# Performance work log

Hardware: AMD Instinct MI355X
Metric: run time of the kernel (lower is better)

## Reference

```python
import jax, jax.numpy as jnp
import numpy as np

B, S, D, K, N = 4, 4096, 768, 24, 8192

def setup_inputs() -> dict:
    key = jax.random.key(0)
    k1, k2, k3, k4 = jax.random.split(key, 4)
    x = jax.random.normal(k1, (B, S, D), dtype=jnp.float32)
    phi = jax.random.normal(k2, (S, K), dtype=jnp.float32)
    M_inputs = jax.random.normal(k3, (D, D), dtype=jnp.float32) / np.sqrt(D)
    M_filters = jax.random.normal(k4, (K, D), dtype=jnp.float32) / np.sqrt(K)
    return {"x": x, "phi": phi, "M_inputs": M_inputs, "M_filters": M_filters, "n": N}


def reference(x, phi, M_inputs, M_filters, n):
    # STU.forward with use_approx=True, use_flash_fft=False
    bsz, sl, d = x.shape
    x_proj = x @ M_inputs               # [B, S, D]
    phi_proj = phi @ M_filters          # [S, D]
    # alternating sign sequence for the 'minus' spectral branch
    sgn = jnp.ones((1, sl, 1), dtype=x.dtype).at[:, 1::2].set(-1.0)
    # filters: [1, S, D, 1] broadcast over the plus/minus stack
    v = phi_proj[None, :, :, None]
    V = jnp.fft.rfft(v, n=n, axis=1)    # [1, n//2+1, D, 1] complex
    U = jnp.stack([x_proj, x_proj * sgn], axis=-1)  # [B, S, D, 2]
    Uf = jnp.fft.rfft(U, n=n, axis=1)   # [B, n//2+1, D, 2]
    U_conv = jnp.fft.irfft(V * Uf, n=n, axis=1)[:, :sl]  # [B, S, D, 2]
    spectral_plus = U_conv[..., 0]
    spectral_minus = U_conv[..., 1] * sgn
    return spectral_plus + spectral_minus
```

## Files before the change

### kernel.cpp

```cpp
#include <hip/hip_runtime.h>
#include <hip/hip_bf16.h>


#define NB 4
#define NS 4096
#define ND 768
#define NK 24

typedef __attribute__((ext_vector_type(8))) short short8;
typedef __attribute__((ext_vector_type(4))) float f32x4;
typedef __attribute__((ext_vector_type(4))) unsigned short u16x4;

static __device__ __forceinline__ float bf2f(unsigned short u) {
  union { unsigned int i; float f; } v; v.i = ((unsigned int)u) << 16; return v.f;
}
static __device__ __forceinline__ unsigned short f2bf(float f) {
  union { float f; unsigned int i; } v; v.f = f;
  return (unsigned short)((v.i + 0x7fffu + ((v.i >> 16) & 1u)) >> 16);
}

__device__ __forceinline__ float2 cadd(float2 a, float2 b){ return make_float2(a.x+b.x, a.y+b.y); }
__device__ __forceinline__ float2 csub(float2 a, float2 b){ return make_float2(a.x-b.x, a.y-b.y); }
__device__ __forceinline__ float2 cmul(float2 a, float2 b){ return make_float2(a.x*b.x-a.y*b.y, a.x*b.y+a.y*b.x); }
__device__ __forceinline__ float2 cmulc(float2 a, float2 b){ return make_float2(a.x*b.x+a.y*b.y, a.y*b.x-a.x*b.y); }

#define C4 0.70710678118654752f
#define C8 0.92387953251128674f
#define S8 0.38268343236508977f
#define TWO_PI 6.28318530717958648f

__device__ __forceinline__ void fft16_dif(float2 v[16]) {
  const float twr[8] = {1.f, C8, C4, S8, 0.f, -S8, -C4, -C8};
  const float twi[8] = {0.f, -S8, -C4, -C8, -1.f, -C8, -C4, -S8};
#pragma unroll
  for (int i = 0; i < 8; ++i) {
    float2 a = v[i], b = v[i+8];
    v[i] = cadd(a, b);
    float2 d = csub(a, b);
    v[i+8] = make_float2(d.x*twr[i]-d.y*twi[i], d.x*twi[i]+d.y*twr[i]);
  }
#pragma unroll
  for (int blk = 0; blk < 16; blk += 8)
#pragma unroll
    for (int i = 0; i < 4; ++i) {
      float2 a = v[blk+i], b = v[blk+i+4];
      v[blk+i] = cadd(a, b);
      float2 d = csub(a, b);
      v[blk+i+4] = make_float2(d.x*twr[2*i]-d.y*twi[2*i], d.x*twi[2*i]+d.y*twr[2*i]);
    }
#pragma unroll
  for (int blk = 0; blk < 16; blk += 4) {
    { float2 a = v[blk],   b = v[blk+2]; v[blk] = cadd(a,b);   v[blk+2] = csub(a,b); }
    { float2 a = v[blk+1], b = v[blk+3]; float2 d = csub(a,b);
      v[blk+1] = cadd(a,b); v[blk+3] = make_float2(d.y, -d.x); }
  }
#pragma unroll
  for (int blk = 0; blk < 16; blk += 2) {
    float2 a = v[blk], b = v[blk+1];
    v[blk] = cadd(a, b); v[blk+1] = csub(a, b);
  }
}

__device__ __forceinline__ void fft16_dif_zero8(float2 v[16]) {
  const float twr[8] = {1.f, C8, C4, S8, 0.f, -S8, -C4, -C8};
  const float twi[8] = {0.f, -S8, -C4, -C8, -1.f, -C8, -C4, -S8};
#pragma unroll
  for (int i = 1; i < 8; ++i) {
    float2 a = v[i];
    v[i+8] = make_float2(a.x*twr[i]-a.y*twi[i], a.x*twi[i]+a.y*twr[i]);
  }
  v[8] = v[0];
#pragma unroll
  for (int blk = 0; blk < 16; blk += 8)
#pragma unroll
    for (int i = 0; i < 4; ++i) {
      float2 a = v[blk+i], b = v[blk+i+4];
      v[blk+i] = cadd(a, b);
      float2 d = csub(a, b);
      v[blk+i+4] = make_float2(d.x*twr[2*i]-d.y*twi[2*i], d.x*twi[2*i]+d.y*twr[2*i]);
    }
#pragma unroll
  for (int blk = 0; blk < 16; blk += 4) {
    { float2 a = v[blk],   b = v[blk+2]; v[blk] = cadd(a,b);   v[blk+2] = csub(a,b); }
    { float2 a = v[blk+1], b = v[blk+3]; float2 d = csub(a,b);
      v[blk+1] = cadd(a,b); v[blk+3] = make_float2(d.y, -d.x); }
  }
#pragma unroll
  for (int blk = 0; blk < 16; blk += 2) {
    float2 a = v[blk], b = v[blk+1];
    v[blk] = cadd(a, b); v[blk+1] = csub(a, b);
  }
}

__device__ __forceinline__ void idft16(float2 v[16]) {
  const float twr[8] = {1.f, C8, C4, S8, 0.f, -S8, -C4, -C8};
  const float twi[8] = {0.f, S8, C4, C8, 1.f, C8, C4, S8};
#pragma unroll
  for (int blk = 0; blk < 16; blk += 2) {
    float2 a = v[blk], b = v[blk+1];
    v[blk] = cadd(a, b); v[blk+1] = csub(a, b);
  }
#pragma unroll
  for (int blk = 0; blk < 16; blk += 4) {
    { float2 a = v[blk],   b = v[blk+2]; v[blk] = cadd(a,b);   v[blk+2] = csub(a,b); }
    { float2 a = v[blk+1], b = v[blk+3]; float2 t = make_float2(-b.y, b.x);
      v[blk+1] = cadd(a,t); v[blk+3] = csub(a,t); }
  }
#pragma unroll
  for (int blk = 0; blk < 16; blk += 8)
#pragma unroll
    for (int i = 0; i < 4; ++i) {
      float2 b = v[blk+i+4];
      float2 t = make_float2(b.x*twr[2*i]-b.y*twi[2*i], b.x*twi[2*i]+b.y*twr[2*i]);
      float2 a = v[blk+i];
      v[blk+i] = cadd(a, t); v[blk+i+4] = csub(a, t);
    }
#pragma unroll
  for (int i = 0; i < 8; ++i) {
    float2 b = v[i+8];
    float2 t = make_float2(b.x*twr[i]-b.y*twi[i], b.x*twi[i]+b.y*twr[i]);
    float2 a = v[i];
    v[i] = cadd(a, t); v[i+8] = csub(a, t);
  }
}

__device__ __forceinline__ void idft16_low8(float2 v[16]) {
  const float twr[8] = {1.f, C8, C4, S8, 0.f, -S8, -C4, -C8};
  const float twi[8] = {0.f, S8, C4, C8, 1.f, C8, C4, S8};
#pragma unroll
  for (int blk = 0; blk < 16; blk += 2) {
    float2 a = v[blk], b = v[blk+1];
    v[blk] = cadd(a, b); v[blk+1] = csub(a, b);
  }
#pragma unroll
  for (int blk = 0; blk < 16; blk += 4) {
    { float2 a = v[blk],   b = v[blk+2]; v[blk] = cadd(a,b);   v[blk+2] = csub(a,b); }
    { float2 a = v[blk+1], b = v[blk+3]; float2 t = make_float2(-b.y, b.x);
      v[blk+1] = cadd(a,t); v[blk+3] = csub(a,t); }
  }
#pragma unroll
  for (int blk = 0; blk < 16; blk += 8)
#pragma unroll
    for (int i = 0; i < 4; ++i) {
      float2 b = v[blk+i+4];
      float2 t = make_float2(b.x*twr[2*i]-b.y*twi[2*i], b.x*twi[2*i]+b.y*twr[2*i]);
      float2 a = v[blk+i];
      v[blk+i] = cadd(a, t); v[blk+i+4] = csub(a, t);
    }
#pragma unroll
  for (int i = 0; i < 8; ++i) {
    float2 b = v[i+8];
    float2 t = make_float2(b.x*twr[i]-b.y*twi[i], b.x*twi[i]+b.y*twr[i]);
    v[i] = cadd(v[i], t);
  }
}

#define BR_TABLE {0,8,4,12,2,10,6,14,1,9,5,13,3,11,7,15}
#define PAD(i) ((i) + ((i) >> 4))

__global__ __launch_bounds__(256) void cast_x_bf16(const float* __restrict__ in,
                                                   unsigned short* __restrict__ out) {
  int i = (blockIdx.x * 256 + threadIdx.x) * 4;
  float4 v = *(const float4*)(in + i);
  u16x4 o = { f2bf(v.x), f2bf(v.y), f2bf(v.z), f2bf(v.w) };
  *(u16x4*)(out + i) = o;
}

__global__ __launch_bounds__(256) void transpose_cast_Mi(const float* __restrict__ Mi,
                                                         unsigned short* __restrict__ MiT) {
  __shared__ float tile[64][65];
  const int d0 = blockIdx.x * 64;
  const int e0 = blockIdx.y * 64;
  const int tid = threadIdx.x;
#pragma unroll
  for (int i = 0; i < 16; ++i) {
    int ee = (tid >> 6) + i * 4;
    int dd = tid & 63;
    tile[ee][dd] = Mi[(e0 + ee) * ND + d0 + dd];
  }
  __syncthreads();
#pragma unroll
  for (int i = 0; i < 8; ++i) {
    int dd = (tid >> 5) + i * 8;
    int ee2 = (tid & 31) * 2;
    unsigned int w = (unsigned int)f2bf(tile[ee2][dd]) |
                     ((unsigned int)f2bf(tile[ee2 + 1][dd]) << 16);
    *(unsigned int*)(MiT + (size_t)(d0 + dd) * ND + e0 + ee2) = w;
  }
}

__global__ __launch_bounds__(256) void gemm_xprojT(const unsigned short* __restrict__ Xb,
                                                   const unsigned short* __restrict__ MiT,
                                                   unsigned short* __restrict__ XPT) {
  __shared__ __align__(16) unsigned char smem[33792];
  unsigned short* As = (unsigned short*)smem;
  unsigned short* Bs = As + 128 * 32;
  const int tid = threadIdx.x;
  const int lane = tid & 63;
  const int wave = tid >> 6;
  const int c0 = blockIdx.x * 128;
  const int r0 = blockIdx.y * 128;
  const int wr = (wave >> 1) * 64;
  const int wc = (wave & 1) * 64;

  f32x4 acc[4][4];
#pragma unroll
  for (int m = 0; m < 4; ++m)
#pragma unroll
    for (int n = 0; n < 4; ++n) acc[m][n] = (f32x4){0.f, 0.f, 0.f, 0.f};

  const int ldRow = (lane >> 2);
  const int ldK = (lane & 3) * 8;

  for (int k0 = 0; k0 < ND; k0 += 32) {
    if (k0) __syncthreads();
#pragma unroll
    for (int h = 0; h < 2; ++h) {
      int c = wave * 2 + h;
      int row = c * 16 + ldRow;
      const unsigned short* ga = Xb + (size_t)(r0 + row) * ND + k0 + ldK;
      const unsigned short* gb = MiT + (size_t)(c0 + row) * ND + k0 + ldK;
      __builtin_amdgcn_global_load_lds(
          (const __attribute__((address_space(1))) void*)ga,
          (__attribute__((address_space(3))) void*)(As + c * 512), 16, 0, 0);
      __builtin_amdgcn_global_load_lds(
          (const __attribute__((address_space(1))) void*)gb,
          (__attribute__((address_space(3))) void*)(Bs + c * 512), 16, 0, 0);
    }
    __syncthreads();

    short8 a[4], b[4];
#pragma unroll
    for (int m = 0; m < 4; ++m)
      a[m] = *(const short8*)(As + (wr + m * 16 + (lane & 15)) * 32 + (lane >> 4) * 8);
#pragma unroll
    for (int n = 0; n < 4; ++n)
      b[n] = *(const short8*)(Bs + (wc + n * 16 + (lane & 15)) * 32 + (lane >> 4) * 8);
#pragma unroll
    for (int m = 0; m < 4; ++m)
#pragma unroll
      for (int n = 0; n < 4; ++n)
        acc[m][n] = __builtin_amdgcn_mfma_f32_16x16x32_bf16(a[m], b[n], acc[m][n], 0, 0, 0);
  }

  __syncthreads();
  unsigned int* Cb = (unsigned int*)smem;
#pragma unroll
  for (int m = 0; m < 4; ++m)
#pragma unroll
    for (int n = 0; n < 4; ++n) {
      int col = wc + n * 16 + (lane & 15);
      int sp = (wr + m * 16 + (lane >> 4) * 4) >> 1;
      f32x4 a4 = acc[m][n];
      unsigned int w0 = (unsigned int)f2bf(a4[0]) | ((unsigned int)f2bf(a4[1]) << 16);
      unsigned int w1 = (unsigned int)f2bf(a4[2]) | ((unsigned int)f2bf(a4[3]) << 16);
      *(uint2*)(Cb + col * 66 + sp) = make_uint2(w0, w1);
    }
  __syncthreads();
  const int bI = r0 >> 12;
  const int sBase = r0 & (NS - 1);
  {
    int col = tid >> 1, half = tid & 1;
    const unsigned int* srcl = Cb + col * 66 + half * 32;
    unsigned int* dstg = (unsigned int*)(XPT + ((size_t)bI * ND + c0 + col) * NS + sBase) + half * 32;
#pragma unroll
    for (int k = 0; k < 8; ++k)
      *(uint4*)(dstg + k * 4) = *(const uint4*)(srcl + k * 4);
  }
}

__global__ __launch_bounds__(256) void filter_fft(const float* __restrict__ phi,
                                                  const float* __restrict__ Mf,
                                                  float2* __restrict__ Hbr) {
  __shared__ float LR[4352], LI[4352];
  __shared__ float2 TA[256], TB[256];
  const int d = blockIdx.x;
  const int tid = threadIdx.x;
  const int BR[16] = BR_TABLE;
  float2 v[16];

  {
    float sn, cs;
    __sincosf(-(TWO_PI / 4096.f) * (float)tid, &sn, &cs); TA[tid] = make_float2(cs, sn);
    __sincosf(-(TWO_PI / 256.f) * (float)tid, &sn, &cs);  TB[tid] = make_float2(cs, sn);
  }

  float mf[NK];
#pragma unroll
  for (int k = 0; k < NK; ++k) mf[k] = Mf[k * ND + d];
#pragma unroll
  for (int n2 = 0; n2 < 8; ++n2) {
    int m = n2 * 256 + tid;
    const float* pr = phi + (size_t)(2 * m) * NK;
    float acc = 0.f;
#pragma unroll
    for (int k = 0; k < NK; ++k) acc += pr[k] * mf[k];
    v[n2] = make_float2(acc, 0.f);
  }
#pragma unroll
  for (int n2 = 8; n2 < 16; ++n2) v[n2] = make_float2(0.f, 0.f);

  fft16_dif_zero8(v);
  __syncthreads();
  const int t1 = tid >> 4, t0 = tid & 15;
#pragma unroll
  for (int p = 1; p < 16; ++p) v[BR[p]] = cmul(v[BR[p]], cmul(TB[p * t1], TA[p * t0]));
#pragma unroll
  for (int r = 0; r < 16; ++r) { int i = BR[r] * 256 + tid; int s = PAD(i); LR[s] = v[r].x; LI[s] = v[r].y; }
  __syncthreads();

  const int p2 = tid >> 4, n0 = tid & 15;
#pragma unroll
  for (int n1 = 0; n1 < 16; ++n1) { int i = p2 * 256 + n1 * 16 + n0; int s = PAD(i); v[n1] = make_float2(LR[s], LI[s]); }
  fft16_dif(v);
#pragma unroll
  for (int p = 1; p < 16; ++p) v[BR[p]] = cmul(v[BR[p]], TB[p * n0]);
  __syncthreads();
#pragma unroll
  for (int r = 0; r < 16; ++r) { int i = p2 * 256 + BR[r] * 16 + n0; int s = PAD(i); LR[s] = v[r].x; LI[s] = v[r].y; }
  __syncthreads();

#pragma unroll
  for (int q = 0; q < 16; ++q) { int i = tid * 16 + q; int s = PAD(i); v[q] = make_float2(LR[s], LI[s]); }
  fft16_dif(v);
  const float sc = 2.0f / 4096.0f;
  float2* H = Hbr + (size_t)d * 4096;
#pragma unroll
  for (int r = 0; r < 16; ++r)
    H[r * 256 + tid] = make_float2(v[r].x * sc, v[r].y * sc);
}

__global__ __launch_bounds__(256) void conv_kernel(const unsigned short* __restrict__ XPT,
                                                   const float2* __restrict__ Hbr,
                                                   unsigned int* __restrict__ outTb) {
  __shared__ float LR[4352], LI[4352];
  __shared__ float2 TA[256], TB[256];
  const int bd = blockIdx.x;
  const int d = bd % ND;
  const int tid = threadIdx.x;
  const int BR[16] = BR_TABLE;
  float2 v[16];

  {
    float sn, cs;
    __sincosf(-(TWO_PI / 4096.f) * (float)tid, &sn, &cs); TA[tid] = make_float2(cs, sn);
    __sincosf(-(TWO_PI / 256.f) * (float)tid, &sn, &cs);  TB[tid] = make_float2(cs, sn);
  }

  const unsigned int* src = (const unsigned int*)(XPT + (size_t)bd * NS);
#pragma unroll
  for (int n2 = 0; n2 < 8; ++n2) {
    unsigned int w = src[n2 * 256 + tid];
    v[n2] = make_float2(bf2f((unsigned short)(w & 0xffffu)), bf2f((unsigned short)(w >> 16)));
  }
#pragma unroll
  for (int n2 = 8; n2 < 16; ++n2) v[n2] = make_float2(0.f, 0.f);

  fft16_dif_zero8(v);
  __syncthreads();
  const int t1 = tid >> 4, t0 = tid & 15;
#pragma unroll
  for (int p = 1; p < 16; ++p) v[BR[p]] = cmul(v[BR[p]], cmul(TB[p * t1], TA[p * t0]));
#pragma unroll
  for (int r = 0; r < 16; ++r) { int i = BR[r] * 256 + tid; int s = PAD(i); LR[s] = v[r].x; LI[s] = v[r].y; }
  __syncthreads();

  const int p2 = tid >> 4, n0 = tid & 15;
#pragma unroll
  for (int n1 = 0; n1 < 16; ++n1) { int i = p2 * 256 + n1 * 16 + n0; int s = PAD(i); v[n1] = make_float2(LR[s], LI[s]); }
  fft16_dif(v);
#pragma unroll
  for (int p = 1; p < 16; ++p) v[BR[p]] = cmul(v[BR[p]], TB[p * n0]);
  __syncthreads();
#pragma unroll
  for (int r = 0; r < 16; ++r) { int i = p2 * 256 + BR[r] * 16 + n0; int s = PAD(i); LR[s] = v[r].x; LI[s] = v[r].y; }
  __syncthreads();

#pragma unroll
  for (int q = 0; q < 16; ++q) { int i = tid * 16 + q; int s = PAD(i); v[q] = make_float2(LR[s], LI[s]); }
  fft16_dif(v);
  const float2* H = Hbr + (size_t)d * 4096;
#pragma unroll
  for (int r = 0; r < 16; ++r) v[r] = cmul(v[r], H[r * 256 + tid]);
  idft16(v);
#pragma unroll
  for (int n = 1; n < 16; ++n) v[n] = cmulc(v[n], TB[n * (tid & 15)]);
#pragma unroll
  for (int n = 0; n < 16; ++n) { int i = tid * 16 + n; int s = PAD(i); LR[s] = v[n].x; LI[s] = v[n].y; }
  __syncthreads();

#pragma unroll
  for (int r = 0; r < 16; ++r) { int i = p2 * 256 + BR[r] * 16 + n0; int s = PAD(i); v[r] = make_float2(LR[s], LI[s]); }
  idft16(v);
  {
    float2 cA = TA[p2 * n0];
#pragma unroll
    for (int n = 0; n < 16; ++n) v[n] = cmulc(v[n], cmul(TB[p2 * n], cA));
  }
  __syncthreads();
#pragma unroll
  for (int n = 0; n < 16; ++n) { int i = p2 * 256 + n * 16 + n0; int s = PAD(i); LR[s] = v[n].x; LI[s] = v[n].y; }
  __syncthreads();

#pragma unroll
  for (int r = 0; r < 16; ++r) { int i = BR[r] * 256 + tid; int s = PAD(i); v[r] = make_float2(LR[s], LI[s]); }
  idft16_low8(v);
  unsigned int* dst = outTb + (size_t)bd * 2048;
#pragma unroll
  for (int n2 = 0; n2 < 8; ++n2) {
    float2 y = v[n2];
    unsigned int w = (unsigned int)f2bf(y.x) | ((unsigned int)f2bf(y.y) << 16);
    dst[(n2 << 8) + tid] = w;
  }
}

__global__ __launch_bounds__(256) void transpose_out(const unsigned int* __restrict__ outTb,
                                                     float* __restrict__ out) {
  __shared__ float tile[64][65];
  const int b = blockIdx.z;
  const int d0 = blockIdx.y * 64;
  const int s0 = blockIdx.x * 64;
  const int tid = threadIdx.x;
#pragma unroll
  for (int i = 0; i < 8; ++i) {
    int dd = (tid >> 5) + i * 8;
    int ss2 = (tid & 31) * 2;
    unsigned int w = outTb[(((size_t)b * ND + d0 + dd) * NS + s0 + ss2) >> 1];
    tile[dd][ss2]     = bf2f((unsigned short)(w & 0xffffu));
    tile[dd][ss2 + 1] = bf2f((unsigned short)(w >> 16));
  }
  __syncthreads();
#pragma unroll
  for (int i = 0; i < 16; ++i) {
    int ss = (tid >> 6) + i * 4;
    int dd = tid & 63;
    out[((size_t)b * NS + s0 + ss) * ND + d0 + dd] = tile[dd][ss];
  }
}

extern "C" void kernel_launch(void* const* d_in, const int* in_sizes, int n_in,
                              void* d_out, int out_size, void* d_ws, size_t ws_size,
                              hipStream_t stream) {
  const float* x   = (const float*)d_in[0];
  const float* phi = (const float*)d_in[1];
  const float* Mi  = (const float*)d_in[2];
  const float* Mf  = (const float*)d_in[3];
  float* out = (float*)d_out;

  const size_t SZ_XPT = (size_t)NB * ND * NS * 2;
  const size_t SZ_HBR = (size_t)ND * 4096 * 8;
  const size_t SZ_POOL = (size_t)NB * ND * NS * 4;
  if (ws_size < SZ_XPT + SZ_HBR + SZ_POOL) return;

  char* ws = (char*)d_ws;
  unsigned short* xprojT = (unsigned short*)ws;
  float2* Hbr = (float2*)(ws + SZ_XPT);
  char* pool = ws + SZ_XPT + SZ_HBR;
  unsigned short* xbf = (unsigned short*)pool;
  unsigned int* outTb = (unsigned int*)pool;
  unsigned short* MiT = (unsigned short*)(pool + 25165824);

  cast_x_bf16<<<(NB * NS * ND) / (256 * 4), 256, 0, stream>>>(x, xbf);
  transpose_cast_Mi<<<dim3(ND / 64, ND / 64), 256, 0, stream>>>(Mi, MiT);
  gemm_xprojT<<<dim3(ND / 128, (NB * NS) / 128), 256, 0, stream>>>(xbf, MiT, xprojT);
  filter_fft<<<ND, 256, 0, stream>>>(phi, Mf, Hbr);
  conv_kernel<<<NB * ND, 256, 0, stream>>>(xprojT, Hbr, outTb);
  transpose_out<<<dim3(NS / 64, ND / 64, NB), 256, 0, stream>>>(outTb, out);
}
```

Measured before the change: 135.5 us.

## Fuse x bf16 cast into GEMM with double-buffered LDS and tile swizzle

Removes the separate cast_x_bf16 kernel. The GEMM now reads fp32 x directly, converts it to bf16 in registers and stores it to LDS. The k-loop becomes double-buffered, so the next tile's global loads overlap the current MFMA work, and a 1D grid with a swizzled block order is meant to improve L2 reuse. This saves one kernel launch and a full write and re-read of the bf16 copy of x. In exchange, the GEMM reads twice as many bytes for A and does the conversion work inside its loop.

```diff
diff --git a/kernel.cpp b/kernel.cpp
--- a/kernel.cpp
+++ b/kernel.cpp
@@ -157,14 +157,6 @@
 
 #define BR_TABLE {0,8,4,12,2,10,6,14,1,9,5,13,3,11,7,15}
 #define PAD(i) ((i) + ((i) >> 4))
-
-__global__ __launch_bounds__(256) void cast_x_bf16(const float* __restrict__ in,
-                                                   unsigned short* __restrict__ out) {
-  int i = (blockIdx.x * 256 + threadIdx.x) * 4;
-  float4 v = *(const float4*)(in + i);
-  u16x4 o = { f2bf(v.x), f2bf(v.y), f2bf(v.z), f2bf(v.w) };
-  *(u16x4*)(out + i) = o;
-}
 
 __global__ __launch_bounds__(256) void transpose_cast_Mi(const float* __restrict__ Mi,
                                                          unsigned short* __restrict__ MiT) {
@@ -189,62 +181,117 @@
   }
 }
 
-__global__ __launch_bounds__(256) void gemm_xprojT(const unsigned short* __restrict__ Xb,
+__global__ __launch_bounds__(256) void gemm_xprojT(const float* __restrict__ Xf,
                                                    const unsigned short* __restrict__ MiT,
                                                    unsigned short* __restrict__ XPT) {
   __shared__ __align__(16) unsigned char smem[33792];
-  unsigned short* As = (unsigned short*)smem;
-  unsigned short* Bs = As + 128 * 32;
+  unsigned short* As0 = (unsigned short*)smem;
+  unsigned short* Bs0 = As0 + 4096;
+  unsigned short* As1 = Bs0 + 4096;
+  unsigned short* Bs1 = As1 + 4096;
+
   const int tid = threadIdx.x;
   const int lane = tid & 63;
   const int wave = tid >> 6;
-  const int c0 = blockIdx.x * 128;
-  const int r0 = blockIdx.y * 128;
+  const int f = blockIdx.x;
+  const int swz = (f & 7) * 96 + (f >> 3);
+  const int c0 = (swz % 6) * 128;
+  const int r0 = (swz / 6) * 128;
+
+  const int rowA = tid >> 2;
+  const int colq = (tid & 3) * 8;
+
+  f32x4 acc[4][4];
+#pragma unroll
+  for (int m = 0; m < 4; ++m)
+#pragma unroll
+    for (int n = 0; n < 4; ++n) acc[m][n] = (f32x4){0.f, 0.f, 0.f, 0.f};
+
+  {
+    const float* ga = Xf + (size_t)(r0 + rowA) * ND + colq;
+    float4 p0 = *(const float4*)ga, p1 = *(const float4*)(ga + 4);
+    const float* ga2 = ga + (size_t)64 * ND;
+    float4 p2 = *(const float4*)ga2, p3 = *(const float4*)(ga2 + 4);
+#pragma unroll
+    for (int h = 0; h < 2; ++h) {
+      int c = wave * 2 + h;
+      int rowc = c * 16 + (lane >> 2);
+      const unsigned short* gb = MiT + (size_t)(c0 + rowc) * ND + (lane & 3) * 8;
+      __builtin_amdgcn_global_load_lds(
+          (const __attribute__((address_space(1))) void*)gb,
+          (__attribute__((address_space(3))) void*)(Bs0 + c * 512), 16, 0, 0);
+    }
+    unsigned int w0 = (unsigned int)f2bf(p0.x) | ((unsigned int)f2bf(p0.y) << 16);
+    unsigned int w1 = (unsigned int)f2bf(p0.z) | ((unsigned int)f2bf(p0.w) << 16);
+    unsigned int w2 = (unsigned int)f2bf(p1.x) | ((unsigned int)f2bf(p1.y) << 16);
+    unsigned int w3 = (unsigned int)f2bf(p1.z) | ((unsigned int)f2bf(p1.w) << 16);
+    *(uint4*)(As0 + tid * 8) = make_uint4(w0, w1, w2, w3);
+    w0 = (unsigned int)f2bf(p2.x) | ((unsigned int)f2bf(p2.y) << 16);
+    w1 = (unsigned int)f2bf(p2.z) | ((unsigned int)f2bf(p2.w) << 16);
+    w2 = (unsigned int)f2bf(p3.x) | ((unsigned int)f2bf(p3.y) << 16);
+    w3 = (unsigned int)f2bf(p3.z) | ((unsigned int)f2bf(p3.w) << 16);
+    *(uint4*)(As0 + 2048 + tid * 8) = make_uint4(w0, w1, w2, w3);
+  }
+  __syncthreads();
+
+  for (int t = 0; t < NK; ++t) {
+    unsigned short* Ac = (t & 1) ? As1 : As0;
+    unsigned short* Bc = (t & 1) ? Bs1 : Bs0;
+    unsigned short* An = (t & 1) ? As0 : As1;
+    unsigned short* Bn = (t & 1) ? Bs0 : Bs1;
+    const bool pre = (t < NK - 1);
+    float4 p0, p1, p2, p3;
+    if (pre) {
+      const int k0n = (t + 1) * 32;
+      const float* ga = Xf + (size_t)(r0 + rowA) * ND + k0n + colq;
+      p0 = *(const float4*)ga; p1 = *(const float4*)(ga + 4);
+      const float* ga2 = ga + (size_t)64 * ND;
+      p2 = *(const float4*)ga2; p3 = *(const float4*)(ga2 + 4);
+#pragma unroll
+      for (int h = 0; h < 2; ++h) {
+        int c = wave * 2 + h;
+        int rowc = c * 16 + (lane >> 2);
+        const unsigned short* gb = MiT + (size_t)(c0 + rowc) * ND + k0n + (lane & 3) * 8;
+        __builtin_amdgcn_global_load_lds(
+            (const __attribute__((address_space(1))) void*)gb,
+            (__attribute__((address_space(3))) void*)(Bn + c * 512), 16, 0, 0);
+      }
+    }
+
+    const int wr = (wave >> 1) * 64;
+    const int wc = (wave & 1) * 64;
+    short8 a[4], b[4];
+#pragma unroll
+    for (int m = 0; m < 4; ++m)
+      a[m] = *(const short8*)(Ac + (wr + m * 16 + (lane & 15)) * 32 + (lane >> 4) * 8);
+#pragma unroll
+    for (int n = 0; n < 4; ++n)
+      b[n] = *(const short8*)(Bc + (wc + n * 16 + (lane & 15)) * 32 + (lane >> 4) * 8);
+#pragma unroll
+    for (int m = 0; m < 4; ++m)
+#pragma unroll
+      for (int n = 0; n < 4; ++n)
+        acc[m][n] = __builtin_amdgcn_mfma_f32_16x16x32_bf16(a[m], b[n], acc[m][n], 0, 0, 0);
+
+    if (pre) {
+      unsigned int w0 = (unsigned int)f2bf(p0.x) | ((unsigned int)f2bf(p0.y) << 16);
+      unsigned int w1 = (unsigned int)f2bf(p0.z) | ((unsigned int)f2bf(p0.w) << 16);
+      unsigned int w2 = (unsigned int)f2bf(p1.x) | ((unsigned int)f2bf(p1.y) << 16);
+      unsigned int w3 = (unsigned int)f2bf(p1.z) | ((unsigned int)f2bf(p1.w) << 16);
+      *(uint4*)(An + tid * 8) = make_uint4(w0, w1, w2, w3);
+      w0 = (unsigned int)f2bf(p2.x) | ((unsigned int)f2bf(p2.y) << 16);
+      w1 = (unsigned int)f2bf(p2.z) | ((unsigned int)f2bf(p2.w) << 16);
+      w2 = (unsigned int)f2bf(p3.x) | ((unsigned int)f2bf(p3.y) << 16);
+      w3 = (unsigned int)f2bf(p3.z) | ((unsigned int)f2bf(p3.w) << 16);
+      *(uint4*)(An + 2048 + tid * 8) = make_uint4(w0, w1, w2, w3);
+      __syncthreads();
+    }
+  }
+  __syncthreads();
+
+  unsigned int* Cb = (unsigned int*)smem;
   const int wr = (wave >> 1) * 64;
   const int wc = (wave & 1) * 64;
-
-  f32x4 acc[4][4];
-#pragma unroll
-  for (int m = 0; m < 4; ++m)
-#pragma unroll
-    for (int n = 0; n < 4; ++n) acc[m][n] = (f32x4){0.f, 0.f, 0.f, 0.f};
-
-  const int ldRow = (lane >> 2);
-  const int ldK = (lane & 3) * 8;
-
-  for (int k0 = 0; k0 < ND; k0 += 32) {
-    if (k0) __syncthreads();
-#pragma unroll
-    for (int h = 0; h < 2; ++h) {
-      int c = wave * 2 + h;
-      int row = c * 16 + ldRow;
-      const unsigned short* ga = Xb + (size_t)(r0 + row) * ND + k0 + ldK;
-      const unsigned short* gb = MiT + (size_t)(c0 + row) * ND + k0 + ldK;
-      __builtin_amdgcn_global_load_lds(
-          (const __attribute__((address_space(1))) void*)ga,
-          (__attribute__((address_space(3))) void*)(As + c * 512), 16, 0, 0);
-      __builtin_amdgcn_global_load_lds(
-          (const __attribute__((address_space(1))) void*)gb,
-          (__attribute__((address_space(3))) void*)(Bs + c * 512), 16, 0, 0);
-    }
-    __syncthreads();
-
-    short8 a[4], b[4];
-#pragma unroll
-    for (int m = 0; m < 4; ++m)
-      a[m] = *(const short8*)(As + (wr + m * 16 + (lane & 15)) * 32 + (lane >> 4) * 8);
-#pragma unroll
-    for (int n = 0; n < 4; ++n)
-      b[n] = *(const short8*)(Bs + (wc + n * 16 + (lane & 15)) * 32 + (lane >> 4) * 8);
-#pragma unroll
-    for (int m = 0; m < 4; ++m)
-#pragma unroll
-      for (int n = 0; n < 4; ++n)
-        acc[m][n] = __builtin_amdgcn_mfma_f32_16x16x32_bf16(a[m], b[n], acc[m][n], 0, 0, 0);
-  }
-
-  __syncthreads();
-  unsigned int* Cb = (unsigned int*)smem;
 #pragma unroll
   for (int m = 0; m < 4; ++m)
 #pragma unroll
@@ -456,13 +503,11 @@
   unsigned short* xprojT = (unsigned short*)ws;
   float2* Hbr = (float2*)(ws + SZ_XPT);
   char* pool = ws + SZ_XPT + SZ_HBR;
-  unsigned short* xbf = (unsigned short*)pool;
   unsigned int* outTb = (unsigned int*)pool;
   unsigned short* MiT = (unsigned short*)(pool + 25165824);
 
-  cast_x_bf16<<<(NB * NS * ND) / (256 * 4), 256, 0, stream>>>(x, xbf);
   transpose_cast_Mi<<<dim3(ND / 64, ND / 64), 256, 0, stream>>>(Mi, MiT);
-  gemm_xprojT<<<dim3(ND / 128, (NB * NS) / 128), 256, 0, stream>>>(xbf, MiT, xprojT);
+  gemm_xprojT<<<768, 256, 0, stream>>>(x, MiT, xprojT);
   filter_fft<<<ND, 256, 0, stream>>>(phi, Mf, Hbr);
   conv_kernel<<<NB * ND, 256, 0, stream>>>(xprojT, Hbr, outTb);
   transpose_out<<<dim3(NS / 64, ND / 64, NB), 256, 0, stream>>>(outTb, out);
```

After: 126.2 us. 1.07x faster.
